# Performance work log

Hardware: AMD Instinct MI355X
Metric: run time of the kernel (lower is better)

## Reference

```python
import jax, jax.numpy as jnp
import numpy as np

NUM_C = 100
DIM_S = 128
SIZE_M = 64
EMB = 128
MAX_CODE_LEN = 128
NODE_COUNT = 10000
PATH_COUNT = 10000
B, L = 16, 128


def setup_inputs() -> dict:
    key = jax.random.key(0)
    ks = jax.random.split(key, 24)
    def nrm(k, shape, fan):
        return jax.random.normal(k, shape, jnp.float32) * np.float32(np.sqrt(2.0 / fan))
    code = jax.random.randint(ks[0], (B, L, NUM_C * 2 + MAX_CODE_LEN * 3), 0, 10000)
    q = jax.random.randint(ks[1], (B, L), 0, NUM_C)
    r = jax.random.randint(ks[2], (B, L), 0, 2 * NUM_C)
    return {
        "code": code, "q": q, "r": r,
        "embed_nodes": nrm(ks[3], (NODE_COUNT + 2, EMB), EMB),
        "embed_paths": nrm(ks[4], (PATH_COUNT + 2, EMB), EMB),
        "W_pt": nrm(ks[5], (3 * EMB, 3 * EMB), 3 * EMB), "b_pt": jnp.zeros((3 * EMB,), jnp.float32),
        "W_att": nrm(ks[6], (3 * EMB, 1), 3 * EMB), "b_att": jnp.zeros((1,), jnp.float32),
        "k_emb": nrm(ks[7], (NUM_C + 1, DIM_S), DIM_S),
        "Mk": nrm(ks[8], (SIZE_M, DIM_S), DIM_S),
        "Mv0": nrm(ks[9], (SIZE_M, DIM_S), DIM_S),
        "v_emb": nrm(ks[10], (NUM_C * 2 + 2, DIM_S), DIM_S),
        "W_e": nrm(ks[11], (4 * DIM_S, DIM_S), 4 * DIM_S), "b_e": jnp.zeros((DIM_S,), jnp.float32),
        "W_a": nrm(ks[12], (4 * DIM_S, DIM_S), 4 * DIM_S), "b_a": jnp.zeros((DIM_S,), jnp.float32),
        "W_f": nrm(ks[13], (2 * DIM_S, DIM_S), 2 * DIM_S), "b_f": jnp.zeros((DIM_S,), jnp.float32),
        "W_p": nrm(ks[14], (DIM_S, 10), DIM_S), "b_p": jnp.zeros((10,), jnp.float32),
    }


def reference(code, q, r, embed_nodes, embed_paths, W_pt, b_pt, W_att, b_att,
              k_emb, Mk, Mv0, v_emb, W_e, b_e, W_a, b_a, W_f, b_f, W_p, b_p):
    bsz = code.shape[0]
    k = k_emb[q]                                    # [B,L,D]
    vr = v_emb[r]                                   # [B,L,D]
    # code2vec path triples: [B,L,MAX_CODE_LEN,3] = (start, path, end)
    c2v = code[:, :, NUM_C * 2:].reshape(bsz, code.shape[1], MAX_CODE_LEN, 3)
    full = jnp.concatenate([embed_nodes[c2v[..., 0]],
                            embed_nodes[c2v[..., 2]],
                            embed_paths[c2v[..., 1]]], axis=3)   # [B,L,P,3E]
    tr = jnp.tanh(full @ W_pt + b_pt)
    cw = tr @ W_att + b_att                          # [B,L,P,1]
    attn = jax.nn.softmax(cw, axis=1)                # faithful: softmax over seq dim (dim=1)
    code_vec = jnp.sum(full * attn, axis=2)          # [B,L,3E]
    v = jnp.concatenate([vr, code_vec], axis=2)      # [B,L,4D]
    w = jax.nn.softmax(k @ Mk.T, axis=-1)            # [B,L,M]
    e = jax.nn.sigmoid(v @ W_e + b_e)                # [B,L,D]
    a = jnp.tanh(v @ W_a + b_a)                      # [B,L,D]
    Mvt0 = jnp.broadcast_to(Mv0, (bsz,) + Mv0.shape) # [B,M,D]

    def step(Mvt, inp):
        et, at, wt = inp                             # [B,D],[B,D],[B,M]
        read = jnp.einsum('bm,bmd->bd', wt, Mvt)     # read pre-update memory (Mv[:, :-1])
        Mvt = Mvt * (1.0 - wt[:, :, None] * et[:, None, :]) + wt[:, :, None] * at[:, None, :]
        return Mvt, read

    _, reads = jax.lax.scan(step, Mvt0,
                            (e.transpose(1, 0, 2), a.transpose(1, 0, 2), w.transpose(1, 0, 2)))
    read = reads.transpose(1, 0, 2)                  # [B,L,D]
    f = jnp.tanh(jnp.concatenate([read, k], axis=-1) @ W_f + b_f)
    # dropout is identity in eval mode
    return jax.nn.sigmoid(f @ W_p + b_p)             # [B,L,10]
```

## Files before the change

### kernel.cpp

```cpp
#include <hip/hip_runtime.h>


typedef unsigned char u8;
typedef unsigned short u16;
typedef unsigned int u32;
typedef __attribute__((ext_vector_type(8))) short short8;
typedef __attribute__((ext_vector_type(4))) float f32x4;
typedef __attribute__((ext_vector_type(2))) float f32x2;

#define DEV __device__ __forceinline__
#define LOG2E 1.4426950408889634f
#define KSCALE 2.8853900817779268f

DEV u16 f2b(float f) {
    union { float f; u32 i; } v; v.f = f;
    u32 x = v.i;
    u32 r = (x + 0x7FFFu + ((x >> 16) & 1u)) >> 16;
    return (u16)r;
}
DEV float nexp(float x) { return __builtin_amdgcn_exp2f(x * LOG2E); }
DEV float nrcp(float x) { return __builtin_amdgcn_rcpf(x); }
DEV float fast_tanh(float x) {
    return 1.f - 2.f * nrcp(1.f + __builtin_amdgcn_exp2f(x * (2.f * LOG2E)));
}
DEV float sigmoidf_(float x) { return nrcp(1.f + __builtin_amdgcn_exp2f(-x * LOG2E)); }
DEV f32x2 d8(u32 x, bool hi) {
    return hi ? __builtin_amdgcn_cvt_pk_f32_fp8((int)x, true)
              : __builtin_amdgcn_cvt_pk_f32_fp8((int)x, false);
}
DEV u8 e8(float x) {
    return (u8)(__builtin_amdgcn_cvt_pk_fp8_f32(x, x, 0, false) & 0xFF);
}

__global__ void k_conv(const float* __restrict__ EN, const float* __restrict__ EP,
                       const float* __restrict__ Wpt, const float* __restrict__ We,
                       const float* __restrict__ Wa, const float* __restrict__ Wf,
                       const float* __restrict__ Wp,
                       const float* __restrict__ Kemb, const float* __restrict__ Mk,
                       u16* __restrict__ ENb, u16* __restrict__ EPb,
                       u8* __restrict__ EN8, u8* __restrict__ EP8,
                       u16* __restrict__ Wt, u16* __restrict__ WeaT,
                       u16* __restrict__ WfT, u16* __restrict__ WpT,
                       float* __restrict__ wsmall) {
    if (blockIdx.x >= 2048) {
        int wv = threadIdx.x >> 6, lane = threadIdx.x & 63;
        int row = (blockIdx.x - 2048) * 4 + wv;
        if (row >= 101) return;
        float lg = 0.f;
        for (int k = 0; k < 128; k += 8) {
            float mk8[8];
#pragma unroll
            for (int u = 0; u < 8; u++) mk8[u] = Mk[lane * 128 + k + u];
#pragma unroll
            for (int u = 0; u < 8; u++) lg = fmaf(Kemb[row * 128 + k + u], mk8[u], lg);
        }
        float mx = lg;
#pragma unroll
        for (int off = 32; off; off >>= 1) mx = fmaxf(mx, __shfl_xor(mx, off, 64));
        float ex = nexp(lg - mx);
        float sum = ex;
#pragma unroll
        for (int off = 32; off; off >>= 1) sum += __shfl_xor(sum, off, 64);
        wsmall[row * 64 + lane] = ex * nrcp(sum);
        return;
    }
    const int NEH = 10002 * 64;
    const int T0 = 2 * NEH;
    const int T1 = T0 + 147456;
    const int T2 = T1 + 131072;
    const int T3 = T2 + 32768;
    const int T4 = T3 + 2048;
    for (int i = blockIdx.x * blockDim.x + threadIdx.x; i < T4; i += 2048 * blockDim.x) {
        if (i < NEH) {
            float a = EN[2 * i], b = EN[2 * i + 1];
            ((u32*)ENb)[i] = ((u32)f2b(b) << 16) | f2b(a);
            ((u16*)EN8)[i] = (u16)__builtin_amdgcn_cvt_pk_fp8_f32(a, b, 0, false);
        } else if (i < T0) {
            int j = i - NEH;
            float a = EP[2 * j], b = EP[2 * j + 1];
            ((u32*)EPb)[j] = ((u32)f2b(b) << 16) | f2b(a);
            ((u16*)EP8)[j] = (u16)__builtin_amdgcn_cvt_pk_fp8_f32(a, b, 0, false);
        } else if (i < T1) {
            int w = i - T0;  u32 n = (u32)w / 384u, k = (u32)w % 384u;
            Wt[w] = f2b(Wpt[k * 384 + n]);
        } else if (i < T2) {
            int w = i - T1;  int n = w >> 9, k = w & 511;
            WeaT[w] = f2b((n < 128) ? We[k * 128 + n] : Wa[k * 128 + (n - 128)]);
        } else if (i < T3) {
            int w = i - T2;  int n = w >> 8, k = w & 255;
            WfT[w] = f2b(Wf[k * 128 + n]);
        } else {
            int w = i - T3;  int n = w >> 7, k = w & 127;
            WpT[w] = (n < 10) ? f2b(Wp[k * 10 + n]) : (u16)0;
        }
    }
}

__global__ void k_preM(const u16* __restrict__ ENb, const u16* __restrict__ EPb,
                       const u16* __restrict__ Wt, const float* __restrict__ bpt,
                       u8* __restrict__ PS8, u8* __restrict__ PE8, u8* __restrict__ PP8) {
    int which = blockIdx.y;
    int r0 = blockIdx.x * 16;
    int wv = threadIdx.x >> 6, lane = threadIdx.x & 63;
    int m = lane & 15, quad = lane >> 4;
    const u16* A = (which == 2) ? EPb : ENb;
    int koff = which * 128;
    u8* dst = (which == 0) ? PS8 : (which == 1) ? PE8 : PP8;

    const short8* ap = (const short8*)(A + (r0 + m) * 128 + quad * 8);
    short8 a0 = ap[0], a1 = ap[4], a2 = ap[8], a3 = ap[12];

    for (int nt = 0; nt < 6; nt++) {
        int n0 = wv * 96 + nt * 16;
        const short8* bp = (const short8*)(Wt + (n0 + m) * 384 + koff + quad * 8);
        f32x4 acc = {0.f, 0.f, 0.f, 0.f};
        acc = __builtin_amdgcn_mfma_f32_16x16x32_bf16(a0, bp[0],  acc, 0, 0, 0);
        acc = __builtin_amdgcn_mfma_f32_16x16x32_bf16(a1, bp[4],  acc, 0, 0, 0);
        acc = __builtin_amdgcn_mfma_f32_16x16x32_bf16(a2, bp[8],  acc, 0, 0, 0);
        acc = __builtin_amdgcn_mfma_f32_16x16x32_bf16(a3, bp[12], acc, 0, 0, 0);
        int col = n0 + m;
        float bias = (which == 2) ? bpt[col] : 0.f;
#pragma unroll
        for (int reg = 0; reg < 4; reg++) {
            int row = r0 + quad * 4 + reg;
            if (row < 10002) dst[row * 384 + col] = e8((acc[reg] + bias) * KSCALE);
        }
    }
}

__global__ void k_cw(const int* __restrict__ code,
                     const u8* __restrict__ PS8, const u8* __restrict__ PE8,
                     const u8* __restrict__ PP8, const float* __restrict__ Watt,
                     float* __restrict__ cw) {
    int wv = threadIdx.x >> 6, lane = threadIdx.x & 63;
    int t0 = (blockIdx.x * 4 + wv) * 8;
    int b = t0 >> 14;
    int rem = t0 & 16383;
    int l = rem >> 7, p0 = rem & 127;

    const int* c = code + ((b * 128 + l) * 584 + 200 + 3 * p0);
    int si[8], pi[8], ei[8];
#pragma unroll
    for (int i = 0; i < 8; i++) {
        si[i] = __builtin_amdgcn_readfirstlane(c[3 * i]);
        pi[i] = __builtin_amdgcn_readfirstlane(c[3 * i + 1]);
        ei[i] = __builtin_amdgcn_readfirstlane(c[3 * i + 2]);
    }

    int j0 = 6 * lane;
    int o32 = j0 + ((lane & 1) << 1);
    int o16 = j0 + ((~lane & 1) << 2);
    float wa0 = -2.f * Watt[o32],     wa1 = -2.f * Watt[o32 + 1];
    float wa2 = -2.f * Watt[o32 + 2], wa3 = -2.f * Watt[o32 + 3];
    float wb0 = -2.f * Watt[o16],     wb1 = -2.f * Watt[o16 + 1];

    u32 xs[8], ys[8], xe[8], ye[8], xq[8], yq[8];
#pragma unroll
    for (int i = 0; i < 8; i++) {
        const u8* bs = PS8 + si[i] * 384;
        const u8* be = PE8 + ei[i] * 384;
        const u8* bq = PP8 + pi[i] * 384;
        xs[i] = *(const u32*)(bs + o32); ys[i] = *(const u16*)(bs + o16);
        xe[i] = *(const u32*)(be + o32); ye[i] = *(const u16*)(be + o16);
        xq[i] = *(const u32*)(bq + o32); yq[i] = *(const u16*)(bq + o16);
    }

#pragma unroll
    for (int i = 0; i < 8; i++) {
        f32x2 zA = d8(xs[i], false) + d8(xe[i], false) + d8(xq[i], false);
        f32x2 zB = d8(xs[i], true)  + d8(xe[i], true)  + d8(xq[i], true);
        f32x2 zC = d8(ys[i], false) + d8(ye[i], false) + d8(yq[i], false);

        float acc = nrcp(1.f + __builtin_amdgcn_exp2f(zA.x)) * wa0;
        acc = fmaf(nrcp(1.f + __builtin_amdgcn_exp2f(zA.y)), wa1, acc);
        acc = fmaf(nrcp(1.f + __builtin_amdgcn_exp2f(zB.x)), wa2, acc);
        acc = fmaf(nrcp(1.f + __builtin_amdgcn_exp2f(zB.y)), wa3, acc);
        acc = fmaf(nrcp(1.f + __builtin_amdgcn_exp2f(zC.x)), wb0, acc);
        acc = fmaf(nrcp(1.f + __builtin_amdgcn_exp2f(zC.y)), wb1, acc);

#pragma unroll
        for (int off = 32; off; off >>= 1) acc += __shfl_down(acc, off, 64);
        if (lane == 0) cw[(b * 128 + p0 + i) * 128 + l] = acc;
    }
}

__global__ void k_sm(const float* __restrict__ cw, float* __restrict__ attn) {
    int b = blockIdx.x >> 3, p0 = (blockIdx.x & 7) * 16;
    int tid = threadIdx.x;
    int wv = tid >> 6, lane = tid & 63;
    __shared__ float tile[16][128];
    __shared__ float atile[128][17];
    for (int idx = tid; idx < 2048; idx += 256) {
        int pp = idx >> 7, l = idx & 127;
        tile[pp][l] = cw[(b * 128 + p0 + pp) * 128 + l];
    }
    __syncthreads();
#pragma unroll
    for (int pl = 0; pl < 4; pl++) {
        int pp = wv * 4 + pl;
        float x0 = tile[pp][lane], x1 = tile[pp][64 + lane];
        float mx = fmaxf(x0, x1);
#pragma unroll
        for (int off = 32; off; off >>= 1) mx = fmaxf(mx, __shfl_xor(mx, off, 64));
        float e0 = nexp(x0 - mx), e1 = nexp(x1 - mx);
        float sum = e0 + e1;
#pragma unroll
        for (int off = 32; off; off >>= 1) sum += __shfl_xor(sum, off, 64);
        float inv = nrcp(sum);
        atile[lane][pp] = e0 * inv;
        atile[64 + lane][pp] = e1 * inv;
    }
    __syncthreads();
    for (int idx = tid; idx < 2048; idx += 256) {
        int l = idx >> 4, pp = idx & 15;
        attn[(b * 128 + l) * 128 + p0 + pp] = atile[l][pp];
    }
}

__global__ void k_cv(const int* __restrict__ code, const float* __restrict__ attn,
                     const u8* __restrict__ EN8, const u8* __restrict__ EP8,
                     const int* __restrict__ rr, const int* __restrict__ qq,
                     const float* __restrict__ Vemb, const float* __restrict__ Kemb,
                     u16* __restrict__ vA, u16* __restrict__ fA) {
    int row = blockIdx.x;
    int tid = threadIdx.x;
    int wv = tid >> 6, lane = tid & 63;
    __shared__ int si[128], ei[128], pi[128];
    __shared__ float at[128];
    __shared__ float part[4][3][128];
    if (tid < 128) {
        const int* c = code + (row * 584 + 200);
        si[tid] = c[3 * tid]; pi[tid] = c[3 * tid + 1]; ei[tid] = c[3 * tid + 2];
        at[tid] = attn[row * 128 + tid];
    }
    if (tid < 128) {
        vA[row * 512 + tid] = f2b(Vemb[rr[row] * 128 + tid]);
    } else {
        int t2 = tid - 128;
        fA[row * 256 + 128 + t2] = f2b(Kemb[qq[row] * 128 + t2]);
    }
    __syncthreads();
    float a0 = 0.f, a1 = 0.f, b0 = 0.f, b1 = 0.f, c0 = 0.f, c1 = 0.f;
    int o = 2 * lane;
    for (int p = wv; p < 128; p += 8) {
        int p2 = p + 4;
        float w = at[p], w2 = at[p2];
        u32 us = *(const u16*)(EN8 + si[p] * 128 + o);
        u32 ue = *(const u16*)(EN8 + ei[p] * 128 + o);
        u32 up = *(const u16*)(EP8 + pi[p] * 128 + o);
        u32 vs = *(const u16*)(EN8 + si[p2] * 128 + o);
        u32 ve = *(const u16*)(EN8 + ei[p2] * 128 + o);
        u32 vp = *(const u16*)(EP8 + pi[p2] * 128 + o);
        f32x2 fs = d8(us, false), fe = d8(ue, false), fp = d8(up, false);
        f32x2 gs = d8(vs, false), ge = d8(ve, false), gp = d8(vp, false);
        a0 = fmaf(w, fs.x, a0); a1 = fmaf(w, fs.y, a1);
        b0 = fmaf(w, fe.x, b0); b1 = fmaf(w, fe.y, b1);
        c0 = fmaf(w, fp.x, c0); c1 = fmaf(w, fp.y, c1);
        a0 = fmaf(w2, gs.x, a0); a1 = fmaf(w2, gs.y, a1);
        b0 = fmaf(w2, ge.x, b0); b1 = fmaf(w2, ge.y, b1);
        c0 = fmaf(w2, gp.x, c0); c1 = fmaf(w2, gp.y, c1);
    }
    part[wv][0][2 * lane] = a0; part[wv][0][2 * lane + 1] = a1;
    part[wv][1][2 * lane] = b0; part[wv][1][2 * lane + 1] = b1;
    part[wv][2][2 * lane] = c0; part[wv][2][2 * lane + 1] = c1;
    __syncthreads();
    u16* vrow = vA + row * 512 + 128;
    for (int idx = tid; idx < 384; idx += 256) {
        int tbl = idx >> 7, col = idx & 127;
        vrow[idx] = f2b(part[0][tbl][col] + part[1][tbl][col] + part[2][tbl][col] + part[3][tbl][col]);
    }
}

__global__ void k_eawM(const u16* __restrict__ vA, const u16* __restrict__ WeaT,
                       const float* __restrict__ be, const float* __restrict__ ba,
                       float* __restrict__ eb, float* __restrict__ ab) {
    int rt = blockIdx.x >> 2, cg = blockIdx.x & 3;
    int wv = threadIdx.x >> 6, lane = threadIdx.x & 63;
    int ct = cg * 4 + wv;
    int m = lane & 15, quad = lane >> 4;
    const short8* ap = (const short8*)(vA + (rt * 16 + m) * 512 + quad * 8);
    const short8* bp = (const short8*)(WeaT + (ct * 16 + m) * 512 + quad * 8);
    f32x4 acc = {0.f, 0.f, 0.f, 0.f};
#pragma unroll
    for (int kc = 0; kc < 16; kc++)
        acc = __builtin_amdgcn_mfma_f32_16x16x32_bf16(ap[kc * 4], bp[kc * 4], acc, 0, 0, 0);
    int col = ct * 16 + m;
    bool isA = col >= 128;
    int c2 = isA ? col - 128 : col;
    float bias = isA ? ba[c2] : be[c2];
#pragma unroll
    for (int reg = 0; reg < 4; reg++) {
        int row = rt * 16 + quad * 4 + reg;
        float val = acc[reg] + bias;
        if (isA) ab[row * 128 + c2] = fast_tanh(val);
        else     eb[row * 128 + c2] = sigmoidf_(val);
    }
}

__global__ void k_scan(const float* __restrict__ Mv0, const float* __restrict__ eb,
                       const float* __restrict__ ab, const float* __restrict__ wsmall,
                       const int* __restrict__ qq, u16* __restrict__ fA) {
    int b = blockIdx.x >> 4, dblk = blockIdx.x & 15;
    int lane = threadIdx.x;
    int s = lane >> 3, dlo = lane & 7;
    int d = dblk * 8 + dlo;

    __shared__ float wsm[101 * 64];
    __shared__ float el[128][8];
    __shared__ float al[128][8];
    __shared__ int ql[128];

    for (int i = lane; i < 101 * 64; i += 64) wsm[i] = wsmall[i];
    for (int i = lane; i < 1024; i += 64) {
        int t = i >> 3, dl = i & 7;
        el[t][dl] = eb[(b * 128 + t) * 128 + dblk * 8 + dl];
        al[t][dl] = ab[(b * 128 + t) * 128 + dblk * 8 + dl];
    }
    for (int i = lane; i < 128; i += 64) ql[i] = qq[b * 128 + i];
    __syncthreads();

    float mv[8];
#pragma unroll
    for (int q = 0; q < 8; q++) mv[q] = Mv0[(s * 8 + q) * 128 + d];

    u16* fout = fA + (b * 128) * 256 + d;

    int qt = ql[0];
    const float4* wr = (const float4*)(wsm + qt * 64 + s * 8);
    float4 w0 = wr[0], w1 = wr[1];
    float ecur = el[0][dlo], acur = al[0][dlo];

    for (int t = 0; t < 128; t++) {
        int tn = (t < 127) ? t + 1 : 127;
        int qn = ql[tn];
        const float4* wrn = (const float4*)(wsm + qn * 64 + s * 8);
        float4 nw0 = wrn[0], nw1 = wrn[1];
        float en = el[tn][dlo], an = al[tn][dlo];

        float w[8] = { w0.x, w0.y, w0.z, w0.w, w1.x, w1.y, w1.z, w1.w };
        float rd = 0.f;
#pragma unroll
        for (int q = 0; q < 8; q++) {
            rd = fmaf(w[q], mv[q], rd);
            mv[q] = fmaf(w[q], fmaf(-mv[q], ecur, acur), mv[q]);
        }
        rd += __shfl_xor(rd, 8, 64);
        rd += __shfl_xor(rd, 16, 64);
        rd += __shfl_xor(rd, 32, 64);
        if (s == 0) fout[t * 256] = f2b(rd);

        ecur = en; acur = an; w0 = nw0; w1 = nw1;
    }
}

__global__ void k_outfin(const u16* __restrict__ fA, const u16* __restrict__ WfT,
                         const float* __restrict__ bfp, const u16* __restrict__ WpT,
                         const float* __restrict__ bp, float* __restrict__ out) {
    int rt = blockIdx.x;
    int wv = threadIdx.x >> 6, lane = threadIdx.x & 63;
    int m = lane & 15, quad = lane >> 4;
    __shared__ u16 ftile[16][128];

    const short8* ap = (const short8*)(fA + (rt * 16 + m) * 256 + quad * 8);
    const short8* bpw = (const short8*)(WfT + (wv * 16 + m) * 256 + quad * 8);
    f32x4 acc = {0.f, 0.f, 0.f, 0.f};
#pragma unroll
    for (int kc = 0; kc < 8; kc++)
        acc = __builtin_amdgcn_mfma_f32_16x16x32_bf16(ap[kc * 4], bpw[kc * 4], acc, 0, 0, 0);
    int col = wv * 16 + m;
    float bias = bfp[col];
#pragma unroll
    for (int reg = 0; reg < 4; reg++)
        ftile[quad * 4 + reg][col] = f2b(fast_tanh(acc[reg] + bias));
    __syncthreads();

    if (wv == 0) {
        f32x4 facc = {0.f, 0.f, 0.f, 0.f};
#pragma unroll
        for (int kc = 0; kc < 4; kc++) {
            short8 af = *(const short8*)(&ftile[m][kc * 32 + quad * 8]);
            short8 bf = *(const short8*)(WpT + m * 128 + kc * 32 + quad * 8);
            facc = __builtin_amdgcn_mfma_f32_16x16x32_bf16(af, bf, facc, 0, 0, 0);
        }
        if (m < 10) {
            float bias2 = bp[m];
#pragma unroll
            for (int reg = 0; reg < 4; reg++) {
                int row = rt * 16 + quad * 4 + reg;
                out[row * 10 + m] = sigmoidf_(facc[reg] + bias2);
            }
        }
    }
}

extern "C" void kernel_launch(void* const* d_in, const int* in_sizes, int n_in,
                              void* d_out, int out_size, void* d_ws, size_t ws_size,
                              hipStream_t stream) {
    const int*   code = (const int*)d_in[0];
    const int*   q    = (const int*)d_in[1];
    const int*   r    = (const int*)d_in[2];
    const float* EN   = (const float*)d_in[3];
    const float* EP   = (const float*)d_in[4];
    const float* Wpt  = (const float*)d_in[5];
    const float* bpt  = (const float*)d_in[6];
    const float* Watt = (const float*)d_in[7];
    const float* Kemb = (const float*)d_in[9];
    const float* Mk   = (const float*)d_in[10];
    const float* Mv0  = (const float*)d_in[11];
    const float* Vemb = (const float*)d_in[12];
    const float* We   = (const float*)d_in[13];
    const float* be   = (const float*)d_in[14];
    const float* Wa   = (const float*)d_in[15];
    const float* ba   = (const float*)d_in[16];
    const float* Wf   = (const float*)d_in[17];
    const float* bf_  = (const float*)d_in[18];
    const float* Wp   = (const float*)d_in[19];
    const float* bp   = (const float*)d_in[20];

    char* ws = (char*)d_ws;
    size_t off = 0;
    auto alloc = [&](size_t bytes) { void* p = ws + off; off = (off + bytes + 255) & ~255UL; return p; };
    u8*    PS8    = (u8*)alloc(10002UL * 384);
    u8*    PE8    = (u8*)alloc(10002UL * 384);
    u8*    PP8    = (u8*)alloc(10002UL * 384);
    u16*   ENb    = (u16*)alloc(10002UL * 128 * 2);
    u16*   EPb    = (u16*)alloc(10016UL * 128 * 2);
    u8*    EN8    = (u8*)alloc(10002UL * 128);
    u8*    EP8    = (u8*)alloc(10002UL * 128);
    u16*   Wt     = (u16*)alloc(384UL * 384 * 2);
    u16*   WeaT   = (u16*)alloc(256UL * 512 * 2);
    u16*   WfT    = (u16*)alloc(128UL * 256 * 2);
    u16*   WpT    = (u16*)alloc(16UL * 128 * 2);
    float* cw     = (float*)alloc(16UL * 128 * 128 * 4);
    float* attn   = (float*)alloc(16UL * 128 * 128 * 4);
    u16*   vA     = (u16*)alloc(2048UL * 512 * 2);
    u16*   fA     = (u16*)alloc(2048UL * 256 * 2);
    float* eb     = (float*)alloc(2048UL * 128 * 4);
    float* ab     = (float*)alloc(2048UL * 128 * 4);
    float* wsmall = (float*)alloc(101UL * 64 * 4);

    k_conv<<<2048 + 26, 256, 0, stream>>>(EN, EP, Wpt, We, Wa, Wf, Wp, Kemb, Mk,
                                          ENb, EPb, EN8, EP8, Wt, WeaT, WfT, WpT, wsmall);
    k_preM<<<dim3(626, 3), 256, 0, stream>>>(ENb, EPb, Wt, bpt, PS8, PE8, PP8);
    k_cw<<<8192, 256, 0, stream>>>(code, PS8, PE8, PP8, Watt, cw);
    k_sm<<<128, 256, 0, stream>>>(cw, attn);
    k_cv<<<2048, 256, 0, stream>>>(code, attn, EN8, EP8, r, q, Vemb, Kemb, vA, fA);
    k_eawM<<<512, 256, 0, stream>>>(vA, WeaT, be, ba, eb, ab);
    k_scan<<<256, 64, 0, stream>>>(Mv0, eb, ab, wsmall, q, fA);
    k_outfin<<<128, 512, 0, stream>>>(fA, WfT, bf_, WpT, bp, (float*)d_out);
}
```

Measured before the change: 258.2 us.

## Widen preM row tiles, vectorize cw gathers, software-pipeline cv gathers

k_preM now computes two 16-row tiles per block so each loaded weight fragment feeds twice as many MFMAs, halving the grid. k_cw switches from per-lane scattered 4+2 byte loads over one path to 16-lane groups each reading 24 contiguous bytes per path, handling 4 paths at once with a 16-lane xor reduction instead of a full 64-lane shuffle chain. k_cv prefetches the next iteration's gathered embeddings while computing the current one. ENb is padded to cover the larger preM tile, at the cost of more registers in all three kernels.

After: 226.2 us. 12.4% less time.

```diff
diff --git a/kernel.cpp b/kernel.cpp
--- a/kernel.cpp
+++ b/kernel.cpp
@@ -100,30 +100,39 @@
                        const u16* __restrict__ Wt, const float* __restrict__ bpt,
                        u8* __restrict__ PS8, u8* __restrict__ PE8, u8* __restrict__ PP8) {
     int which = blockIdx.y;
-    int r0 = blockIdx.x * 16;
+    int r0 = blockIdx.x * 32;
     int wv = threadIdx.x >> 6, lane = threadIdx.x & 63;
     int m = lane & 15, quad = lane >> 4;
     const u16* A = (which == 2) ? EPb : ENb;
     int koff = which * 128;
     u8* dst = (which == 0) ? PS8 : (which == 1) ? PE8 : PP8;
 
-    const short8* ap = (const short8*)(A + (r0 + m) * 128 + quad * 8);
-    short8 a0 = ap[0], a1 = ap[4], a2 = ap[8], a3 = ap[12];
+    short8 a[2][4];
+#pragma unroll
+    for (int rt = 0; rt < 2; rt++) {
+        const short8* ap = (const short8*)(A + (r0 + rt * 16 + m) * 128 + quad * 8);
+#pragma unroll
+        for (int kc = 0; kc < 4; kc++) a[rt][kc] = ap[kc * 4];
+    }
 
     for (int nt = 0; nt < 6; nt++) {
         int n0 = wv * 96 + nt * 16;
         const short8* bp = (const short8*)(Wt + (n0 + m) * 384 + koff + quad * 8);
-        f32x4 acc = {0.f, 0.f, 0.f, 0.f};
-        acc = __builtin_amdgcn_mfma_f32_16x16x32_bf16(a0, bp[0],  acc, 0, 0, 0);
-        acc = __builtin_amdgcn_mfma_f32_16x16x32_bf16(a1, bp[4],  acc, 0, 0, 0);
-        acc = __builtin_amdgcn_mfma_f32_16x16x32_bf16(a2, bp[8],  acc, 0, 0, 0);
-        acc = __builtin_amdgcn_mfma_f32_16x16x32_bf16(a3, bp[12], acc, 0, 0, 0);
+        short8 b0 = bp[0], b1 = bp[4], b2 = bp[8], b3 = bp[12];
         int col = n0 + m;
         float bias = (which == 2) ? bpt[col] : 0.f;
 #pragma unroll
-        for (int reg = 0; reg < 4; reg++) {
-            int row = r0 + quad * 4 + reg;
-            if (row < 10002) dst[row * 384 + col] = e8((acc[reg] + bias) * KSCALE);
+        for (int rt = 0; rt < 2; rt++) {
+            f32x4 acc = {0.f, 0.f, 0.f, 0.f};
+            acc = __builtin_amdgcn_mfma_f32_16x16x32_bf16(a[rt][0], b0, acc, 0, 0, 0);
+            acc = __builtin_amdgcn_mfma_f32_16x16x32_bf16(a[rt][1], b1, acc, 0, 0, 0);
+            acc = __builtin_amdgcn_mfma_f32_16x16x32_bf16(a[rt][2], b2, acc, 0, 0, 0);
+            acc = __builtin_amdgcn_mfma_f32_16x16x32_bf16(a[rt][3], b3, acc, 0, 0, 0);
+#pragma unroll
+            for (int reg = 0; reg < 4; reg++) {
+                int row = r0 + rt * 16 + quad * 4 + reg;
+                if (row < 10002) dst[row * 384 + col] = e8((acc[reg] + bias) * KSCALE);
+            }
         }
     }
 }
@@ -133,6 +142,7 @@
                      const u8* __restrict__ PP8, const float* __restrict__ Watt,
                      float* __restrict__ cw) {
     int wv = threadIdx.x >> 6, lane = threadIdx.x & 63;
+    int g = lane >> 4, gl = lane & 15;
     int t0 = (blockIdx.x * 4 + wv) * 8;
     int b = t0 >> 14;
     int rem = t0 & 16383;
@@ -147,40 +157,48 @@
         ei[i] = __builtin_amdgcn_readfirstlane(c[3 * i + 2]);
     }
 
-    int j0 = 6 * lane;
-    int o32 = j0 + ((lane & 1) << 1);
-    int o16 = j0 + ((~lane & 1) << 2);
-    float wa0 = -2.f * Watt[o32],     wa1 = -2.f * Watt[o32 + 1];
-    float wa2 = -2.f * Watt[o32 + 2], wa3 = -2.f * Watt[o32 + 3];
-    float wb0 = -2.f * Watt[o16],     wb1 = -2.f * Watt[o16 + 1];
-
-    u32 xs[8], ys[8], xe[8], ye[8], xq[8], yq[8];
-#pragma unroll
-    for (int i = 0; i < 8; i++) {
-        const u8* bs = PS8 + si[i] * 384;
-        const u8* be = PE8 + ei[i] * 384;
-        const u8* bq = PP8 + pi[i] * 384;
-        xs[i] = *(const u32*)(bs + o32); ys[i] = *(const u16*)(bs + o16);
-        xe[i] = *(const u32*)(be + o32); ye[i] = *(const u16*)(be + o16);
-        xq[i] = *(const u32*)(bq + o32); yq[i] = *(const u16*)(bq + o16);
-    }
-
-#pragma unroll
-    for (int i = 0; i < 8; i++) {
-        f32x2 zA = d8(xs[i], false) + d8(xe[i], false) + d8(xq[i], false);
-        f32x2 zB = d8(xs[i], true)  + d8(xe[i], true)  + d8(xq[i], true);
-        f32x2 zC = d8(ys[i], false) + d8(ye[i], false) + d8(yq[i], false);
-
-        float acc = nrcp(1.f + __builtin_amdgcn_exp2f(zA.x)) * wa0;
-        acc = fmaf(nrcp(1.f + __builtin_amdgcn_exp2f(zA.y)), wa1, acc);
-        acc = fmaf(nrcp(1.f + __builtin_amdgcn_exp2f(zB.x)), wa2, acc);
-        acc = fmaf(nrcp(1.f + __builtin_amdgcn_exp2f(zB.y)), wa3, acc);
-        acc = fmaf(nrcp(1.f + __builtin_amdgcn_exp2f(zC.x)), wb0, acc);
-        acc = fmaf(nrcp(1.f + __builtin_amdgcn_exp2f(zC.y)), wb1, acc);
-
-#pragma unroll
-        for (int off = 32; off; off >>= 1) acc += __shfl_down(acc, off, 64);
-        if (lane == 0) cw[(b * 128 + p0 + i) * 128 + l] = acc;
+    float w24[24];
+    const float4* wp = (const float4*)(Watt + gl * 24);
+#pragma unroll
+    for (int u = 0; u < 6; u++) {
+        float4 f = wp[u];
+        w24[4 * u + 0] = -2.f * f.x; w24[4 * u + 1] = -2.f * f.y;
+        w24[4 * u + 2] = -2.f * f.z; w24[4 * u + 3] = -2.f * f.w;
+    }
+
+    float res[2];
+#pragma unroll
+    for (int batch = 0; batch < 2; batch++) {
+        int i = batch * 4 + g;
+        const uint2* bs = (const uint2*)(PS8 + si[i] * 384 + gl * 24);
+        const uint2* be = (const uint2*)(PE8 + ei[i] * 384 + gl * 24);
+        const uint2* bq = (const uint2*)(PP8 + pi[i] * 384 + gl * 24);
+        uint2 s0 = bs[0], s1 = bs[1], s2 = bs[2];
+        uint2 e0 = be[0], e1 = be[1], e2 = be[2];
+        uint2 q0 = bq[0], q1 = bq[1], q2 = bq[2];
+
+        float acc = 0.f;
+        u32 sv[6] = { s0.x, s0.y, s1.x, s1.y, s2.x, s2.y };
+        u32 ev[6] = { e0.x, e0.y, e1.x, e1.y, e2.x, e2.y };
+        u32 qv[6] = { q0.x, q0.y, q1.x, q1.y, q2.x, q2.y };
+#pragma unroll
+        for (int u = 0; u < 6; u++) {
+            f32x2 zl = d8(sv[u], false) + d8(ev[u], false) + d8(qv[u], false);
+            f32x2 zh = d8(sv[u], true)  + d8(ev[u], true)  + d8(qv[u], true);
+            acc = fmaf(nrcp(1.f + __builtin_amdgcn_exp2f(zl.x)), w24[4 * u + 0], acc);
+            acc = fmaf(nrcp(1.f + __builtin_amdgcn_exp2f(zl.y)), w24[4 * u + 1], acc);
+            acc = fmaf(nrcp(1.f + __builtin_amdgcn_exp2f(zh.x)), w24[4 * u + 2], acc);
+            acc = fmaf(nrcp(1.f + __builtin_amdgcn_exp2f(zh.y)), w24[4 * u + 3], acc);
+        }
+        acc += __shfl_xor(acc, 1, 64);
+        acc += __shfl_xor(acc, 2, 64);
+        acc += __shfl_xor(acc, 4, 64);
+        acc += __shfl_xor(acc, 8, 64);
+        res[batch] = acc;
+    }
+    if (gl == 0) {
+        cw[(b * 128 + p0 + g) * 128 + l] = res[0];
+        cw[(b * 128 + p0 + 4 + g) * 128 + l] = res[1];
     }
 }
 
@@ -242,23 +260,43 @@
     __syncthreads();
     float a0 = 0.f, a1 = 0.f, b0 = 0.f, b1 = 0.f, c0 = 0.f, c1 = 0.f;
     int o = 2 * lane;
-    for (int p = wv; p < 128; p += 8) {
-        int p2 = p + 4;
-        float w = at[p], w2 = at[p2];
-        u32 us = *(const u16*)(EN8 + si[p] * 128 + o);
-        u32 ue = *(const u16*)(EN8 + ei[p] * 128 + o);
-        u32 up = *(const u16*)(EP8 + pi[p] * 128 + o);
-        u32 vs = *(const u16*)(EN8 + si[p2] * 128 + o);
-        u32 ve = *(const u16*)(EN8 + ei[p2] * 128 + o);
-        u32 vp = *(const u16*)(EP8 + pi[p2] * 128 + o);
-        f32x2 fs = d8(us, false), fe = d8(ue, false), fp = d8(up, false);
-        f32x2 gs = d8(vs, false), ge = d8(ve, false), gp = d8(vp, false);
+
+    u32 cur[6];
+    {
+        int p = wv, p2 = wv + 4;
+        cur[0] = *(const u16*)(EN8 + si[p] * 128 + o);
+        cur[1] = *(const u16*)(EN8 + ei[p] * 128 + o);
+        cur[2] = *(const u16*)(EP8 + pi[p] * 128 + o);
+        cur[3] = *(const u16*)(EN8 + si[p2] * 128 + o);
+        cur[4] = *(const u16*)(EN8 + ei[p2] * 128 + o);
+        cur[5] = *(const u16*)(EP8 + pi[p2] * 128 + o);
+    }
+#pragma unroll
+    for (int it = 0; it < 16; it++) {
+        int p = wv + it * 8;
+        u32 nxt[6];
+        if (it < 15) {
+            int pn = p + 8, pn2 = p + 12;
+            nxt[0] = *(const u16*)(EN8 + si[pn] * 128 + o);
+            nxt[1] = *(const u16*)(EN8 + ei[pn] * 128 + o);
+            nxt[2] = *(const u16*)(EP8 + pi[pn] * 128 + o);
+            nxt[3] = *(const u16*)(EN8 + si[pn2] * 128 + o);
+            nxt[4] = *(const u16*)(EN8 + ei[pn2] * 128 + o);
+            nxt[5] = *(const u16*)(EP8 + pi[pn2] * 128 + o);
+        }
+        float w = at[p], w2 = at[p + 4];
+        f32x2 fs = d8(cur[0], false), fe = d8(cur[1], false), fp = d8(cur[2], false);
+        f32x2 gs = d8(cur[3], false), ge = d8(cur[4], false), gp = d8(cur[5], false);
         a0 = fmaf(w, fs.x, a0); a1 = fmaf(w, fs.y, a1);
         b0 = fmaf(w, fe.x, b0); b1 = fmaf(w, fe.y, b1);
         c0 = fmaf(w, fp.x, c0); c1 = fmaf(w, fp.y, c1);
         a0 = fmaf(w2, gs.x, a0); a1 = fmaf(w2, gs.y, a1);
         b0 = fmaf(w2, ge.x, b0); b1 = fmaf(w2, ge.y, b1);
         c0 = fmaf(w2, gp.x, c0); c1 = fmaf(w2, gp.y, c1);
+        if (it < 15) {
+#pragma unroll
+            for (int z = 0; z < 6; z++) cur[z] = nxt[z];
+        }
     }
     part[wv][0][2 * lane] = a0; part[wv][0][2 * lane + 1] = a1;
     part[wv][1][2 * lane] = b0; part[wv][1][2 * lane + 1] = b1;
@@ -423,7 +461,7 @@
     u8*    PS8    = (u8*)alloc(10002UL * 384);
     u8*    PE8    = (u8*)alloc(10002UL * 384);
     u8*    PP8    = (u8*)alloc(10002UL * 384);
-    u16*   ENb    = (u16*)alloc(10002UL * 128 * 2);
+    u16*   ENb    = (u16*)alloc(10016UL * 128 * 2);
     u16*   EPb    = (u16*)alloc(10016UL * 128 * 2);
     u8*    EN8    = (u8*)alloc(10002UL * 128);
     u8*    EP8    = (u8*)alloc(10002UL * 128);
@@ -441,7 +479,7 @@
 
     k_conv<<<2048 + 26, 256, 0, stream>>>(EN, EP, Wpt, We, Wa, Wf, Wp, Kemb, Mk,
                                           ENb, EPb, EN8, EP8, Wt, WeaT, WfT, WpT, wsmall);
-    k_preM<<<dim3(626, 3), 256, 0, stream>>>(ENb, EPb, Wt, bpt, PS8, PE8, PP8);
+    k_preM<<<dim3(313, 3), 256, 0, stream>>>(ENb, EPb, Wt, bpt, PS8, PE8, PP8);
     k_cw<<<8192, 256, 0, stream>>>(code, PS8, PE8, PP8, Watt, cw);
     k_sm<<<128, 256, 0, stream>>>(cw, attn);
     k_cv<<<2048, 256, 0, stream>>>(code, attn, EN8, EP8, r, q, Vemb, Kemb, vA, fA);
```
